# Performance work log

Measured on AMD Instinct MI355X. Metric: run time of the kernel, lower is better.

The kernel has to match this reference:

```python
import jax, jax.numpy as jnp
import numpy as np

B, L, D = 2, 2048, 2048
H, KV = 32, 8
HD = D // H          # 64
REP = H // KV        # 4


def setup_inputs() -> dict:
    key = jax.random.key(0)
    ks = jax.random.split(key, 6)
    x = jax.random.normal(ks[0], (B, L, D), dtype=jnp.float32)
    # weights stored [in, out] (transpose of torch Linear weight), scaled for stability
    wq = jax.random.normal(ks[1], (D, H * HD), dtype=jnp.float32) * 0.02
    wk = jax.random.normal(ks[2], (D, KV * HD), dtype=jnp.float32) * 0.02
    wv = jax.random.normal(ks[3], (D, KV * HD), dtype=jnp.float32) * 0.02
    wo = jax.random.normal(ks[4], (H * HD, D), dtype=jnp.float32) * 0.02
    # RoPE frequencies: freqs_cis = exp(i * pos * theta), theta_j = 10000^{-2j/HD}
    inv_freq = 1.0 / (10000.0 ** (jnp.arange(0, HD, 2, dtype=jnp.float32) / HD))  # [HD/2]
    angles = jnp.arange(L, dtype=jnp.float32)[:, None] * inv_freq[None, :]        # [L, HD/2]
    freqs_cos = jnp.cos(angles)
    freqs_sin = jnp.sin(angles)
    # additive causal mask [L, L] (prefill from start_pos=0)
    mask = jnp.where(jnp.tril(jnp.ones((L, L), dtype=bool)), 0.0, -jnp.inf).astype(jnp.float32)
    return {"x": x, "start_pos": 0, "freqs_cos": freqs_cos, "freqs_sin": freqs_sin,
            "mask": mask, "wq": wq, "wk": wk, "wv": wv, "wo": wo}


def _apply_rope(t, cos, sin):
    # t: [B, L, h, HD]; cos/sin: [L, HD/2] -> broadcast [1, L, 1, HD/2]
    tp = t.reshape(*t.shape[:-1], HD // 2, 2)
    a, b = tp[..., 0], tp[..., 1]
    c = cos[None, :, None, :]
    s = sin[None, :, None, :]
    ra = a * c - b * s
    rb = a * s + b * c
    return jnp.stack([ra, rb], axis=-1).reshape(t.shape)


def reference(x, start_pos, freqs_cos, freqs_sin, mask, wq, wk, wv, wo):
    xq = jnp.einsum('bld,de->ble', x, wq).reshape(B, L, H, HD)
    xk = jnp.einsum('bld,de->ble', x, wk).reshape(B, L, KV, HD)
    xv = jnp.einsum('bld,de->ble', x, wv).reshape(B, L, KV, HD)
    xq = _apply_rope(xq, freqs_cos, freqs_sin)
    xk = _apply_rope(xk, freqs_cos, freqs_sin)
    # (cache write of xk/xv is a dead side effect in the torch module; omitted)
    # GQA: query head (g*REP + r) attends to kv head g  == repeat_interleave semantics
    q = xq.transpose(0, 2, 1, 3).reshape(B, KV, REP, L, HD)  # [B,KV,REP,L,HD]
    k = xk.transpose(0, 2, 1, 3)                              # [B,KV,L,HD]
    v = xv.transpose(0, 2, 1, 3)
    scale = 1.0 / jnp.sqrt(jnp.float32(HD))
    scores = jnp.einsum('bgrld,bgmd->bgrlm', q, k) * scale + mask  # [B,KV,REP,L,L]
    attn = jax.nn.softmax(scores, axis=-1)
    out = jnp.einsum('bgrlm,bgmd->bgrld', attn, v)            # [B,KV,REP,L,HD]
    out = out.reshape(B, H, L, HD).transpose(0, 2, 1, 3).reshape(B, L, H * HD)
    return jnp.einsum('ble,ed->bld', out, wo)
```

## Files before the change

kernel.cpp:

```cpp
#include <hip/hip_runtime.h>
#include <hip/hip_bf16.h>
#include <math.h>

typedef __bf16 bf16_t;
typedef __bf16 bf16x8 __attribute__((ext_vector_type(8)));
typedef __bf16 bf16x4 __attribute__((ext_vector_type(4)));
typedef __bf16 bf16x2 __attribute__((ext_vector_type(2)));
typedef float  f32x4  __attribute__((ext_vector_type(4)));
typedef int    i32x4  __attribute__((ext_vector_type(4)));

#define B_  2
#define L_  2048
#define D_  2048
#define H_  32
#define KV_ 8
#define HD_ 64

static __device__ __forceinline__ void gload_lds16(const bf16_t* g, void* l)
{
    __builtin_amdgcn_global_load_lds(
        (const __attribute__((address_space(1))) void*)g,
        (__attribute__((address_space(3))) void*)l, 16, 0, 0);
}

static __device__ __forceinline__ int packbf(float a, float b)
{
    bf16x2 t; t[0] = (bf16_t)a; t[1] = (bf16_t)b;
    return __builtin_bit_cast(int, t);
}

static __device__ __forceinline__ void pl32(int& a, int& b)
{
    asm("v_permlane32_swap_b32 %0, %1" : "+v"(a), "+v"(b));
}
static __device__ __forceinline__ void pl16(int& a, int& b)
{
    asm("v_permlane16_swap_b32 %0, %1" : "+v"(a), "+v"(b));
}

#define WAITV4() asm volatile("s_waitcnt vmcnt(4)" ::: "memory")
#define WAITV2() asm volatile("s_waitcnt vmcnt(2)" ::: "memory")
#define WAITV0() asm volatile("s_waitcnt vmcnt(0)" ::: "memory")
#define WAITL0() asm volatile("s_waitcnt lgkmcnt(0)" ::: "memory")

__global__ void cast_f32_bf16(const float4* __restrict__ in,
                              bf16x4* __restrict__ out, int n4)
{
    const int i = blockIdx.x * 256 + threadIdx.x;
    if (i >= n4) return;
    const float4 v = in[i];
    bf16x4 o;
    o[0] = (bf16_t)v.x; o[1] = (bf16_t)v.y; o[2] = (bf16_t)v.z; o[3] = (bf16_t)v.w;
    out[i] = o;
}

template <typename InT>
__global__ void transpose_cast(const InT* __restrict__ in, bf16_t* __restrict__ out,
                               int R, int C)
{
    __shared__ bf16_t tile[32][33];
    const int bx = blockIdx.x * 32, by = blockIdx.y * 32;
    in  += (size_t)blockIdx.z * R * C;
    out += (size_t)blockIdx.z * R * C;
    const int tx = threadIdx.x, ty = threadIdx.y;
#pragma unroll
    for (int i = ty; i < 32; i += 8)
        tile[i][tx] = (bf16_t)(float)in[(size_t)(by + i) * C + bx + tx];
    __syncthreads();
#pragma unroll
    for (int i = ty; i < 32; i += 8)
        out[(size_t)(bx + i) * R + by + tx] = tile[tx][i];
}

#define FRAG(base, row, kk) \
    (*(const bf16x8*)((base) + (size_t)(row) * 128 + ((((kk) * 4 + quad) ^ sw8) << 4)))

#define STG_A(kt, h, buf) do {                                                        \
    gload_lds16(Ag + (size_t)((h) * 128)      * 2048 + (size_t)(kt) * 64,             \
                sdst + (buf) * 32768 + (h) * 16384);                                  \
    gload_lds16(Ag + (size_t)((h) * 128 + 64) * 2048 + (size_t)(kt) * 64,             \
                sdst + (buf) * 32768 + (h) * 16384 + 8192);                           \
} while (0)

#define STG_B(kt, h, buf) do {                                                        \
    gload_lds16(Bg + (size_t)((h) * 128)      * 2048 + (size_t)(kt) * 64,             \
                sdst + 65536 + (buf) * 32768 + (h) * 16384);                          \
    gload_lds16(Bg + (size_t)((h) * 128 + 64) * 2048 + (size_t)(kt) * 64,             \
                sdst + 65536 + (buf) * 32768 + (h) * 16384 + 8192);                   \
} while (0)

#define PHASE_SET(AB, BB, STG1, STG2, STG3, STG4, VM4)                                \
  {                                        \
    _Pragma("unroll") for (int m = 0; m < 4; m++) {                                   \
        Afr[m][0] = FRAG(AB, arow + m * 16, 0);                                       \
        Afr[m][1] = FRAG(AB, arow + m * 16, 1); }                                     \
    _Pragma("unroll") for (int n = 0; n < 2; n++) {                                   \
        B01[n][0] = FRAG(BB, brow + n * 16, 0);                                       \
        B01[n][1] = FRAG(BB, brow + n * 16, 1); }                                     \
    STG1;                                                                             \
    asm volatile("s_waitcnt lgkmcnt(8)" ::: "memory");                                \
    __builtin_amdgcn_s_barrier();                                                     \
    WAITL0();                                                                         \
    __builtin_amdgcn_s_setprio(1);                                                    \
    _Pragma("unroll") for (int m = 0; m < 4; m++)                                     \
      _Pragma("unroll") for (int n = 0; n < 2; n++)                                   \
        _Pragma("unroll") for (int kk = 0; kk < 2; kk++)                              \
          acc[m][n] = __builtin_amdgcn_mfma_f32_16x16x32_bf16(                        \
              Afr[m][kk], B01[n][kk], acc[m][n], 0, 0, 0);                            \
    __builtin_amdgcn_s_setprio(0);                                                    \
    __builtin_amdgcn_s_barrier();                                                     \
  }                                                                                   \
  {                                                 \
    _Pragma("unroll") for (int n = 0; n < 2; n++) {                                   \
        B23[n][0] = FRAG(BB, brow + (n + 2) * 16, 0);                                 \
        B23[n][1] = FRAG(BB, brow + (n + 2) * 16, 1); }                               \
    STG2;                                                                             \
    __builtin_amdgcn_s_barrier();                                                     \
    WAITL0();                                                                         \
    __builtin_amdgcn_s_setprio(1);                                                    \
    _Pragma("unroll") for (int m = 0; m < 4; m++)                                     \
      _Pragma("unroll") for (int n = 0; n < 2; n++)                                   \
        _Pragma("unroll") for (int kk = 0; kk < 2; kk++)                              \
          acc[m][n + 2] = __builtin_amdgcn_mfma_f32_16x16x32_bf16(                    \
              Afr[m][kk], B23[n][kk], acc[m][n + 2], 0, 0, 0);                        \
    __builtin_amdgcn_s_setprio(0);                                                    \
    __builtin_amdgcn_s_barrier();                                                     \
  }                                                                                   \
  {                                                 \
    _Pragma("unroll") for (int m = 0; m < 4; m++) {                                   \
        Afr[m][0] = FRAG(AB, arow + (m + 4) * 16, 0);                                 \
        Afr[m][1] = FRAG(AB, arow + (m + 4) * 16, 1); }                               \
    STG3;                                                                             \
    __builtin_amdgcn_s_barrier();                                                     \
    WAITL0();                                                                         \
    __builtin_amdgcn_s_setprio(1);                                                    \
    _Pragma("unroll") for (int m = 0; m < 4; m++)                                     \
      _Pragma("unroll") for (int n = 0; n < 2; n++)                                   \
        _Pragma("unroll") for (int kk = 0; kk < 2; kk++)                              \
          acc[m + 4][n + 2] = __builtin_amdgcn_mfma_f32_16x16x32_bf16(                \
              Afr[m][kk], B23[n][kk], acc[m + 4][n + 2], 0, 0, 0);                    \
    __builtin_amdgcn_s_setprio(0);                                                    \
    __builtin_amdgcn_s_barrier();                                                     \
  }                                                                                   \
  {                                        \
    STG4;                                                                             \
    VM4;                                                                              \
    __builtin_amdgcn_s_barrier();                                                     \
    __builtin_amdgcn_s_setprio(1);                                                    \
    _Pragma("unroll") for (int m = 0; m < 4; m++)                                     \
      _Pragma("unroll") for (int n = 0; n < 2; n++)                                   \
        _Pragma("unroll") for (int kk = 0; kk < 2; kk++)                              \
          acc[m + 4][n] = __builtin_amdgcn_mfma_f32_16x16x32_bf16(                    \
              Afr[m][kk], B01[n][kk], acc[m + 4][n], 0, 0, 0);                        \
    __builtin_amdgcn_s_setprio(0);                                                    \
    __builtin_amdgcn_s_barrier();                                                     \
  }

__global__ __launch_bounds__(512, 2) void gemm_qkv(
    const bf16_t* __restrict__ A,
    const bf16_t* __restrict__ BT,
    bf16_t* __restrict__ Qb, bf16_t* __restrict__ Kb, bf16_t* __restrict__ Vb)
{
    extern __shared__ __attribute__((aligned(16))) char DLDS[];
    constexpr int NITER = 2048 / 64 / 2;

    const int tid  = threadIdx.x;
    const int wave = tid >> 6;
    const int lane = tid & 63;
    const int quad = lane >> 4;
    const int l16  = lane & 15;
    const int wr   = wave >> 2;
    const int wc   = wave & 3;
    const int m0   = blockIdx.y * 256;
    const int n0   = blockIdx.x * 256;

    const int srow  = tid >> 3;
    const int swcol = ((tid & 7) ^ (srow & 7)) * 8;
    const bf16_t* Ag = A  + (size_t)(m0 + srow) * 2048 + swcol;
    const bf16_t* Bg = BT + (size_t)(n0 + srow) * 2048 + swcol;
    char* sdst = DLDS + tid * 16;

    const char* AB0 = DLDS;
    const char* AB1 = DLDS + 32768;
    const char* BB0 = DLDS + 65536;
    const char* BB1 = DLDS + 98304;
    const int sw8  = l16 & 7;
    const int arow = wr * 128 + l16;
    const int brow = wc * 64 + l16;

    f32x4 acc[8][4];
    const f32x4 zf = {0.f, 0.f, 0.f, 0.f};
#pragma unroll
    for (int i = 0; i < 8; i++)
#pragma unroll
        for (int j = 0; j < 4; j++) acc[i][j] = zf;

    bf16x8 Afr[4][2], B01[2][2], B23[2][2];

    STG_B(0, 0, 0); STG_B(0, 1, 0); STG_A(0, 0, 0); STG_A(0, 1, 0);
    STG_B(1, 0, 1); STG_B(1, 1, 1);
    WAITV4();
    __builtin_amdgcn_s_barrier();

    for (int i = 0; i < NITER; ++i) {
        const int t1 = 2 * i + 1;
        const int t2 = 2 * i + 2;
        const int t3 = 2 * i + 3;
        const bool more = (i + 1 < NITER);

        PHASE_SET(AB0, BB0,
                  STG_A(t1, 0, 1),
                  STG_A(t1, 1, 1),
                  if (more) STG_B(t2, 0, 0),
                  if (more) STG_B(t2, 1, 0),
                  if (more) { WAITV4(); } else { WAITV0(); })
        PHASE_SET(AB1, BB1,
                  if (more) STG_A(t2, 0, 0),
                  if (more) STG_A(t2, 1, 0),
                  if (more) STG_B(t3, 0, 1),
                  if (more) STG_B(t3, 1, 1),
                  WAITV4())
    }

    bf16_t* Cb; int ldc, coff; float cs = 1.f;
    if (n0 < 2048)      { Cb = Qb; ldc = 2048; coff = 0; }
    else if (n0 < 2560) { Cb = Kb; ldc = 512;  coff = 2048;
                          cs = 0.18033688011112042f; }
    else                { Cb = Vb; ldc = 512;  coff = 2560; }

#pragma unroll
    for (int mt = 0; mt < 8; mt++)
#pragma unroll
        for (int nt = 0; nt < 4; nt++)
#pragma unroll
            for (int r = 0; r < 4; r++) {
                const int row = m0 + wr * 128 + mt * 16 + quad * 4 + r;
                const int col = n0 + wc * 64 + nt * 16 + l16 - coff;
                Cb[(size_t)row * ldc + col] = (bf16_t)(acc[mt][nt][r] * cs);
            }
}

#undef FRAG
#undef STG_A
#undef STG_B
#undef PHASE_SET

#define OFRAG(base, row, kk) \
    (*(const bf16x8*)((base) + (size_t)(row) * 128 + ((((kk) * 4 + quad) ^ sw8) << 4)))

#define OSTG_A(kt, h, buf) do {                                                       \
    gload_lds16(Ag + (size_t)((h) * 128)      * 2048 + (size_t)(kt) * 64,             \
                adst + (buf) * 32768 + (h) * 16384);                                  \
    gload_lds16(Ag + (size_t)((h) * 128 + 64) * 2048 + (size_t)(kt) * 64,             \
                adst + (buf) * 32768 + (h) * 16384 + 8192);                           \
} while (0)

#define OSTG_B(kt, buf) do {                                                          \
    gload_lds16(Bg + (size_t)(kt) * 64,                       bdst + (buf) * 16384);  \
    gload_lds16(Bg + (size_t)64 * 2048 + (size_t)(kt) * 64,   bdst + (buf) * 16384 + 8192); \
} while (0)

#define OTILE(AB, BB, SA, SB, VMW)                                                    \
  {                                             \
    _Pragma("unroll") for (int m = 0; m < 4; m++) {                                   \
        Afr[m][0] = OFRAG(AB, arow + m * 16, 0);                                      \
        Afr[m][1] = OFRAG(AB, arow + m * 16, 1); }                                    \
    _Pragma("unroll") for (int n = 0; n < 2; n++) {                                   \
        Bfr[n][0] = OFRAG(BB, brow + n * 16, 0);                                      \
        Bfr[n][1] = OFRAG(BB, brow + n * 16, 1); }                                    \
    SA;                                                                               \
    asm volatile("s_waitcnt lgkmcnt(8)" ::: "memory");                                \
    __builtin_amdgcn_s_barrier();                                                     \
    WAITL0();                                                                         \
    __builtin_amdgcn_s_setprio(1);                                                    \
    _Pragma("unroll") for (int m = 0; m < 4; m++)                                     \
      _Pragma("unroll") for (int n = 0; n < 2; n++)                                   \
        _Pragma("unroll") for (int kk = 0; kk < 2; kk++)                              \
          acc[m][n] = __builtin_amdgcn_mfma_f32_16x16x32_bf16(                        \
              Afr[m][kk], Bfr[n][kk], acc[m][n], 0, 0, 0);                            \
    __builtin_amdgcn_s_setprio(0);                                                    \
    __builtin_amdgcn_s_barrier();                                                     \
  }                                                                                   \
  {                                \
    _Pragma("unroll") for (int m = 0; m < 4; m++) {                                   \
        Afr[m][0] = OFRAG(AB, arow + (m + 4) * 16, 0);                                \
        Afr[m][1] = OFRAG(AB, arow + (m + 4) * 16, 1); }                              \
    SB;                                                                               \
    VMW;                                                                              \
    __builtin_amdgcn_s_barrier();                                                     \
    WAITL0();                                                                         \
    __builtin_amdgcn_s_setprio(1);                                                    \
    _Pragma("unroll") for (int m = 0; m < 4; m++)                                     \
      _Pragma("unroll") for (int n = 0; n < 2; n++)                                   \
        _Pragma("unroll") for (int kk = 0; kk < 2; kk++)                              \
          acc[m + 4][n] = __builtin_amdgcn_mfma_f32_16x16x32_bf16(                    \
              Afr[m][kk], Bfr[n][kk], acc[m + 4][n], 0, 0, 0);                        \
    __builtin_amdgcn_s_setprio(0);                                                    \
    __builtin_amdgcn_s_barrier();                                                     \
  }

__global__ __launch_bounds__(512, 2) void gemm_out(
    const bf16_t* __restrict__ A,
    const bf16_t* __restrict__ BT,
    float* __restrict__ C)
{
    extern __shared__ __attribute__((aligned(16))) char DLDS[];
    constexpr int NITER = 2048 / 64 / 2;

    const int tid  = threadIdx.x;
    const int wave = tid >> 6;
    const int lane = tid & 63;
    const int quad = lane >> 4;
    const int l16  = lane & 15;
    const int wr   = wave >> 2;
    const int wc   = wave & 3;

    const int id   = blockIdx.x;
    const int w    = id >> 3;
    const int m0   = ((id & 7) * 2 + (w & 1)) * 256;
    const int n0   = (w >> 1) * 128;

    const int srow  = tid >> 3;
    const int swcol = ((tid & 7) ^ (srow & 7)) * 8;
    const bf16_t* Ag = A  + (size_t)(m0 + srow) * 2048 + swcol;
    const bf16_t* Bg = BT + (size_t)(n0 + srow) * 2048 + swcol;
    char* adst = DLDS + tid * 16;
    char* bdst = DLDS + 65536 + tid * 16;

    const char* AB0 = DLDS;
    const char* AB1 = DLDS + 32768;
    const char* BB0 = DLDS + 65536;
    const char* BB1 = DLDS + 81920;
    const int sw8  = l16 & 7;
    const int arow = wr * 128 + l16;
    const int brow = wc * 32 + l16;

    f32x4 acc[8][2];
    const f32x4 zf = {0.f, 0.f, 0.f, 0.f};
#pragma unroll
    for (int i = 0; i < 8; i++)
#pragma unroll
        for (int j = 0; j < 2; j++) acc[i][j] = zf;

    bf16x8 Afr[4][2], Bfr[2][2];

    OSTG_B(0, 0); OSTG_A(0, 0, 0); OSTG_A(0, 1, 0); OSTG_B(1, 1);
    WAITV2();
    __builtin_amdgcn_s_barrier();

    for (int i = 0; i < NITER; ++i) {
        const int v  = 2 * i + 1;
        const int t2 = 2 * i + 2;
        const int t3 = 2 * i + 3;
        const bool more = (i + 1 < NITER);

        OTILE(AB0, BB0,
              { OSTG_A(v, 0, 1); OSTG_A(v, 1, 1); },
              { if (more) OSTG_B(t2, 0); },
              if (more) { WAITV2(); } else { WAITV0(); })
        OTILE(AB1, BB1,
              { if (more) { OSTG_A(t2, 0, 0); OSTG_A(t2, 1, 0); } },
              { if (more) OSTG_B(t3, 1); },
              if (more) { WAITV2(); } else { WAITV0(); })
    }

#pragma unroll
    for (int mt = 0; mt < 8; mt++)
#pragma unroll
        for (int nt = 0; nt < 2; nt++)
#pragma unroll
            for (int r = 0; r < 4; r++) {
                const int row = m0 + wr * 128 + mt * 16 + quad * 4 + r;
                const int col = n0 + wc * 32 + nt * 16 + l16;
                C[(size_t)row * 2048 + col] = acc[mt][nt][r];
            }
}

#undef OFRAG
#undef OSTG_A
#undef OSTG_B
#undef OTILE

__global__ void rope_k(bf16_t* __restrict__ T, const float* __restrict__ fc,
                       const float* __restrict__ fs, int nheads, int total8)
{
    const int idx = blockIdx.x * 256 + threadIdx.x;
    if (idx >= total8) return;
    const int g  = idx & 7;
    const int t  = idx >> 3;
    const int h  = t % nheads;
    const int bl = t / nheads;
    const int l  = bl & (L_ - 1);
    const float4 c4 = *(const float4*)(fc + l * 32 + g * 4);
    const float4 s4 = *(const float4*)(fs + l * 32 + g * 4);
    const size_t off = ((size_t)bl * nheads + h) * 64 + g * 8;
    const bf16x8 v = *(const bf16x8*)(T + off);
    const float cc[4] = {c4.x, c4.y, c4.z, c4.w};
    const float ss[4] = {s4.x, s4.y, s4.z, s4.w};
    bf16x8 o;
#pragma unroll
    for (int p = 0; p < 4; p++) {
        const float a  = (float)v[2 * p];
        const float b2 = (float)v[2 * p + 1];
        o[2 * p]     = (bf16_t)(a * cc[p] - b2 * ss[p]);
        o[2 * p + 1] = (bf16_t)(a * ss[p] + b2 * cc[p]);
    }
    *(bf16x8*)(T + off) = o;
}

__global__ __launch_bounds__(256, 2) void attn_k(
    const bf16_t* __restrict__ Q,
    const bf16_t* __restrict__ Kc,
    const bf16_t* __restrict__ VT,
    bf16_t* __restrict__ Ob)
{
    __shared__ __attribute__((aligned(16))) char LDS[32768];
    float* OL = (float*)LDS;
    float* LR = (float*)(LDS + 17408);

    const int tid  = threadIdx.x;
    const int wave = tid >> 6;
    const int lane = tid & 63;
    const int quad = lane >> 4;
    const int l16  = lane & 15;

    const int id   = blockIdx.y * 16 + blockIdx.x;
    const int c    = (id >> 3) & 15;
    const int bh   = (id & 7) * 8 + (id >> 7);
    const int bb   = bh >> 5;
    const int h    = bh & 31;
    const int kvh  = h >> 2;
    const size_t bbL = (size_t)bb * L_;

    const int schunk = ((lane & 3) ^ ((lane >> 3) & 3)) * 8;
    const int sw16   = ((l16 >> 1) & 3) * 16;

    const bf16_t* Kg = Kc + bbL * (KV_ * HD_) + kvh * HD_;
    const bf16_t* Vg = VT + (size_t)(bb * KV_ + kvh) * HD_ * L_;
    const bf16_t* KgL = Kg + (size_t)(wave * 32 + (lane >> 2)) * (KV_ * HD_) + schunk;
    const bf16_t* VgL = Vg + (size_t)(lane >> 2) * L_ + wave * 32 + schunk;
    char* kdst0 = (char*)LDS + wave * 2048 + (lane << 4);
    char* vdst0 = (char*)LDS + 16384 + wave * 4096 + (lane << 4);

    const f32x4 zf = {0.f, 0.f, 0.f, 0.f};

    for (int half = 0; half < 2; ++half) {
        const int j     = half ? c : 31 - c;
        const int qbase = j * 64;
        const int nkt   = (j + 2) >> 1;

        bf16x8 qf[4][2];
#pragma unroll
        for (int qt = 0; qt < 4; qt++) {
            const bf16_t* qrow = Q + ((bbL + qbase + qt * 16 + l16) * H_ + h) * HD_;
            qf[qt][0] = *(const bf16x8*)(qrow + quad * 8);
            qf[qt][1] = *(const bf16x8*)(qrow + 32 + quad * 8);
        }

        f32x4 acc[4][4];
#pragma unroll
        for (int mt = 0; mt < 4; mt++)
#pragma unroll
            for (int qt = 0; qt < 4; qt++) acc[mt][qt] = zf;
        float lacc[4] = {0.f, 0.f, 0.f, 0.f};

#pragma unroll
        for (int cc = 0; cc < 2; cc++)
#pragma unroll
            for (int sub = 0; sub < 2; sub++)
                gload_lds16(KgL + (size_t)(sub * 16) * (KV_ * HD_) + cc * 32,
                            kdst0 + cc * 8192 + sub * 1024);
#pragma unroll
        for (int sub = 0; sub < 4; sub++)
            gload_lds16(VgL + (size_t)(sub * 16) * L_, vdst0 + sub * 1024);

        for (int kt = 0; kt < nkt; kt++) {
            WAITV0();

            const char* Kld = LDS;
            const char* Vld = LDS + 16384;

            bf16x8 kf[2][2];
#pragma unroll
            for (int t = 0; t < 2; t++)
#pragma unroll
                for (int cc = 0; cc < 2; cc++)
                    kf[t][cc] = *(const bf16x8*)(Kld + cc * 8192 +
                        (wave * 32 + t * 16 + l16) * 64 + ((quad * 16) ^ sw16));

            bf16x8 vf[4];
#pragma unroll
            for (int mt = 0; mt < 4; mt++)
                vf[mt] = *(const bf16x8*)(Vld + wave * 4096 +
                    (mt * 16 + l16) * 64 + ((quad * 16) ^ sw16));

            WAITL0();

            if (kt + 1 < nkt) {
                const int ktb = (kt + 1) * 128;
#pragma unroll
                for (int cc = 0; cc < 2; cc++)
#pragma unroll
                    for (int sub = 0; sub < 2; sub++)
                        gload_lds16(KgL + (size_t)(ktb + sub * 16) * (KV_ * HD_) + cc * 32,
                                    kdst0 + cc * 8192 + sub * 1024);
#pragma unroll
                for (int sub = 0; sub < 4; sub++)
                    gload_lds16(VgL + (size_t)(sub * 16) * L_ + ktb,
                                vdst0 + sub * 1024);
            }

            f32x4 st[2][4];
            __builtin_amdgcn_s_setprio(1);
#pragma unroll
            for (int t = 0; t < 2; t++)
#pragma unroll
                for (int qt = 0; qt < 4; qt++) {
                    f32x4 s = __builtin_amdgcn_mfma_f32_16x16x32_bf16(
                        kf[t][0], qf[qt][0], zf, 0, 0, 0);
                    st[t][qt] = __builtin_amdgcn_mfma_f32_16x16x32_bf16(
                        kf[t][1], qf[qt][1], s, 0, 0, 0);
                }
            __builtin_amdgcn_s_setprio(0);

            if (kt == nkt - 1) {
                const int kq = kt * 128 + wave * 32 + quad * 4 - qbase - l16;
#pragma unroll
                for (int t = 0; t < 2; t++)
#pragma unroll
                    for (int qt = 0; qt < 4; qt++)
#pragma unroll
                        for (int r = 0; r < 4; r++)
                            st[t][qt][r] = (kq + t * 16 - qt * 16 + r <= 0)
                                         ? st[t][qt][r] : -__builtin_inff();
            }

            int pk[2][4][2];
#pragma unroll
            for (int t = 0; t < 2; t++)
#pragma unroll
                for (int qt = 0; qt < 4; qt++) {
                    const float e0 = __builtin_amdgcn_exp2f(st[t][qt][0]);
                    const float e1 = __builtin_amdgcn_exp2f(st[t][qt][1]);
                    const float e2 = __builtin_amdgcn_exp2f(st[t][qt][2]);
                    const float e3 = __builtin_amdgcn_exp2f(st[t][qt][3]);
                    lacc[qt] += (e0 + e1) + (e2 + e3);
                    pk[t][qt][0] = packbf(e0, e1);
                    pk[t][qt][1] = packbf(e2, e3);
                }

#pragma unroll
            for (int qt = 0; qt < 4; qt++) {
                int a0 = pk[0][qt][0], b0 = pk[1][qt][0];
                pl32(a0, b0); pl16(a0, b0);
                int a1 = pk[0][qt][1], b1 = pk[1][qt][1];
                pl32(a1, b1); pl16(a1, b1);
                i32x4 bi;
                bi[0] = a0; bi[1] = a1; bi[2] = b0; bi[3] = b1;
                const bf16x8 pb = __builtin_bit_cast(bf16x8, bi);
                __builtin_amdgcn_s_setprio(1);
#pragma unroll
                for (int mt = 0; mt < 4; mt++)
                    acc[mt][qt] = __builtin_amdgcn_mfma_f32_16x16x32_bf16(
                        vf[mt], pb, acc[mt][qt], 0, 0, 0);
                __builtin_amdgcn_s_setprio(0);
            }
        }

        float lw[4];
#pragma unroll
        for (int qt = 0; qt < 4; qt++) {
            float v = lacc[qt];
            v += __shfl_xor(v, 16);
            v += __shfl_xor(v, 32);
            lw[qt] = v;
        }

        __syncthreads();

        if (quad == 0)
#pragma unroll
            for (int qt = 0; qt < 4; qt++)
                LR[(wave * 4 + qt) * 16 + l16] = lw[qt];

#pragma unroll
        for (int p = 0; p < 4; p++) {
#pragma unroll
            for (int qt = 0; qt < 4; qt++) {
                if (((qt - wave) & 3) == p) {
#pragma unroll
                    for (int mt = 0; mt < 4; mt++) {
                        float* a = OL + (qt * 16 + l16) * 68 + mt * 16 + quad * 4;
                        if (p == 0) *(f32x4*)a = acc[mt][qt];
                        else        *(f32x4*)a = *(f32x4*)a + acc[mt][qt];
                    }
                }
            }
            __syncthreads();
        }

        const float ls = LR[(0 * 4 + wave) * 16 + l16] + LR[(1 * 4 + wave) * 16 + l16]
                       + LR[(2 * 4 + wave) * 16 + l16] + LR[(3 * 4 + wave) * 16 + l16];
        const float inv = 1.f / ls;
        bf16_t* orow = Ob + ((bbL + qbase + wave * 16 + l16) * H_ + h) * HD_;
#pragma unroll
        for (int j2 = 0; j2 < 4; j2++) {
            const f32x4 v = *(const f32x4*)(OL + (wave * 16 + l16) * 68 + quad * 16 + j2 * 4);
            bf16x4 o;
#pragma unroll
            for (int i = 0; i < 4; i++) o[i] = (bf16_t)(v[i] * inv);
            *(bf16x4*)(orow + quad * 16 + j2 * 4) = o;
        }
        __syncthreads();
    }
}

extern "C" void kernel_launch(void* const* d_in, const int* in_sizes, int n_in,
                              void* d_out, int out_size, void* d_ws, size_t ws_size,
                              hipStream_t stream)
{
    (void)in_sizes; (void)n_in; (void)out_size; (void)ws_size;
    const float* xf = (const float*)d_in[0];
    const float* fc = (const float*)d_in[2];
    const float* fs = (const float*)d_in[3];
    const float* wq = (const float*)d_in[5];
    const float* wk = (const float*)d_in[6];
    const float* wv = (const float*)d_in[7];
    const float* wo = (const float*)d_in[8];
    float* out = (float*)d_out;

    char* ws = (char*)d_ws;
    bf16_t* xb   = (bf16_t*)(ws);
    bf16_t* Qb   = (bf16_t*)(ws + (16ull << 20));
    bf16_t* Kb   = (bf16_t*)(ws + (32ull << 20));
    bf16_t* Vb   = (bf16_t*)(ws + (36ull << 20));
    bf16_t* VTb  = (bf16_t*)(ws + (40ull << 20));
    bf16_t* Oa   = (bf16_t*)(ws + (44ull << 20));
    bf16_t* Wqkv = (bf16_t*)(ws + (60ull << 20));
    bf16_t* WoT  = (bf16_t*)(ws + (72ull << 20));

    cast_f32_bf16<<<8192, 256, 0, stream>>>((const float4*)xf, (bf16x4*)xb,
                                            B_ * L_ * D_ / 4);

    const dim3 tb(32, 8);
    transpose_cast<float><<<dim3(64, 64, 1), tb, 0, stream>>>(wq, Wqkv, 2048, 2048);
    transpose_cast<float><<<dim3(16, 64, 1), tb, 0, stream>>>(wk, Wqkv + 2048ull * 2048, 2048, 512);
    transpose_cast<float><<<dim3(16, 64, 1), tb, 0, stream>>>(wv, Wqkv + 2560ull * 2048, 2048, 512);
    transpose_cast<float><<<dim3(64, 64, 1), tb, 0, stream>>>(wo, WoT, 2048, 2048);

    gemm_qkv<<<dim3(12, 16), 512, 131072, stream>>>(xb, Wqkv, Qb, Kb, Vb);

    rope_k<<<4096, 256, 0, stream>>>(Qb, fc, fs, 32, B_ * L_ * 32 * 8);
    rope_k<<<1024, 256, 0, stream>>>(Kb, fc, fs, 8, B_ * L_ * 8 * 8);

    transpose_cast<bf16_t><<<dim3(16, 64, 2), tb, 0, stream>>>(Vb, VTb, 2048, 512);

    attn_k<<<dim3(16, 64), 256, 0, stream>>>(Qb, Kb, VTb, Oa);

    gemm_out<<<dim3(256), 512, 98304, stream>>>(Oa, WoT, out);
}
```

Before: 305.0 us.

## Retile QKV GEMM to 256x192 tiles, fuse prep and RoPE launches

The QKV projection GEMM moves from 256x256 tiles on a 12x16 grid (192 blocks) to 256x192 tiles on 256 blocks. The intent is to fill all compute units of the MI355X and cut wave-quantization idle time; the B-operand staging and the LDS size shrink to match. The weight transpose-casts and the x cast are merged into one prep launch, and the Q and K RoPE launches are merged into one, to reduce launch overhead. In exchange, the epilogue now routes each output element to Q, K or V with per-element branching, and the K-scale is applied by column.

```diff
diff --git a/kernel.cpp b/kernel.cpp
--- a/kernel.cpp
+++ b/kernel.cpp
@@ -38,20 +38,49 @@
     asm("v_permlane16_swap_b32 %0, %1" : "+v"(a), "+v"(b));
 }
 
-#define WAITV4() asm volatile("s_waitcnt vmcnt(4)" ::: "memory")
+#define WAITV3() asm volatile("s_waitcnt vmcnt(3)" ::: "memory")
 #define WAITV2() asm volatile("s_waitcnt vmcnt(2)" ::: "memory")
 #define WAITV0() asm volatile("s_waitcnt vmcnt(0)" ::: "memory")
 #define WAITL0() asm volatile("s_waitcnt lgkmcnt(0)" ::: "memory")
 
-__global__ void cast_f32_bf16(const float4* __restrict__ in,
-                              bf16x4* __restrict__ out, int n4)
-{
-    const int i = blockIdx.x * 256 + threadIdx.x;
-    if (i >= n4) return;
-    const float4 v = in[i];
-    bf16x4 o;
-    o[0] = (bf16_t)v.x; o[1] = (bf16_t)v.y; o[2] = (bf16_t)v.z; o[3] = (bf16_t)v.w;
-    out[i] = o;
+__global__ void prep_k(const float* __restrict__ wq, const float* __restrict__ wk,
+                       const float* __restrict__ wv, const float* __restrict__ wo,
+                       const float* __restrict__ xf,
+                       bf16_t* __restrict__ Wqkv, bf16_t* __restrict__ WoT,
+                       bf16_t* __restrict__ xb)
+{
+    __shared__ bf16_t tile[32][33];
+    const int z  = blockIdx.z;
+    const int tx = threadIdx.x, ty = threadIdx.y;
+
+    if (z == 4) {
+        const size_t base = ((size_t)(blockIdx.y * 64 + blockIdx.x) * 256
+                             + ty * 32 + tx) * 8;
+        const float4 v0 = *(const float4*)(xf + base);
+        const float4 v1 = *(const float4*)(xf + base + 4);
+        bf16x8 o;
+        o[0] = (bf16_t)v0.x; o[1] = (bf16_t)v0.y; o[2] = (bf16_t)v0.z; o[3] = (bf16_t)v0.w;
+        o[4] = (bf16_t)v1.x; o[5] = (bf16_t)v1.y; o[6] = (bf16_t)v1.z; o[7] = (bf16_t)v1.w;
+        *(bf16x8*)(xb + base) = o;
+        return;
+    }
+
+    const float* in; bf16_t* out; int C;
+    if (z == 0)      { in = wq; out = Wqkv;                  C = 2048; }
+    else if (z == 1) { in = wk; out = Wqkv + 2048ull * 2048; C = 512;  }
+    else if (z == 2) { in = wv; out = Wqkv + 2560ull * 2048; C = 512;  }
+    else             { in = wo; out = WoT;                   C = 2048; }
+
+    const int bx = blockIdx.x * 32, by = blockIdx.y * 32;
+    if (bx >= C) return;
+    const int R = 2048;
+#pragma unroll
+    for (int i = ty; i < 32; i += 8)
+        tile[i][tx] = (bf16_t)in[(size_t)(by + i) * C + bx + tx];
+    __syncthreads();
+#pragma unroll
+    for (int i = ty; i < 32; i += 8)
+        out[(size_t)(bx + i) * R + by + tx] = tile[tx][i];
 }
 
 template <typename InT>
@@ -82,22 +111,19 @@
                 sdst + (buf) * 32768 + (h) * 16384 + 8192);                           \
 } while (0)
 
-#define STG_B(kt, h, buf) do {                                                        \
-    gload_lds16(Bg + (size_t)((h) * 128)      * 2048 + (size_t)(kt) * 64,             \
-                sdst + 65536 + (buf) * 32768 + (h) * 16384);                          \
-    gload_lds16(Bg + (size_t)((h) * 128 + 64) * 2048 + (size_t)(kt) * 64,             \
-                sdst + 65536 + (buf) * 32768 + (h) * 16384 + 8192);                   \
-} while (0)
-
-#define PHASE_SET(AB, BB, STG1, STG2, STG3, STG4, VM4)                                \
-  {                                        \
+#define STG_BU(kt, u, buf)                                                            \
+    gload_lds16(Bg + (size_t)((u) * 64) * 2048 + (size_t)(kt) * 64,                   \
+                sdst + 65536 + (buf) * 24576 + (u) * 8192)
+
+#define QTILE(AB, BB, S1, S2, S3, S4, VMW)                                            \
+  {                                  \
     _Pragma("unroll") for (int m = 0; m < 4; m++) {                                   \
         Afr[m][0] = FRAG(AB, arow + m * 16, 0);                                       \
         Afr[m][1] = FRAG(AB, arow + m * 16, 1); }                                     \
     _Pragma("unroll") for (int n = 0; n < 2; n++) {                                   \
         B01[n][0] = FRAG(BB, brow + n * 16, 0);                                       \
         B01[n][1] = FRAG(BB, brow + n * 16, 1); }                                     \
-    STG1;                                                                             \
+    S1;                                                                               \
     asm volatile("s_waitcnt lgkmcnt(8)" ::: "memory");                                \
     __builtin_amdgcn_s_barrier();                                                     \
     WAITL0();                                                                         \
@@ -110,41 +136,38 @@
     __builtin_amdgcn_s_setprio(0);                                                    \
     __builtin_amdgcn_s_barrier();                                                     \
   }                                                                                   \
-  {                                                 \
-    _Pragma("unroll") for (int n = 0; n < 2; n++) {                                   \
-        B23[n][0] = FRAG(BB, brow + (n + 2) * 16, 0);                                 \
-        B23[n][1] = FRAG(BB, brow + (n + 2) * 16, 1); }                               \
-    STG2;                                                                             \
+  {                                              \
+    B2f[0] = FRAG(BB, brow + 32, 0);                                                  \
+    B2f[1] = FRAG(BB, brow + 32, 1);                                                  \
+    S2;                                                                               \
     __builtin_amdgcn_s_barrier();                                                     \
     WAITL0();                                                                         \
     __builtin_amdgcn_s_setprio(1);                                                    \
     _Pragma("unroll") for (int m = 0; m < 4; m++)                                     \
-      _Pragma("unroll") for (int n = 0; n < 2; n++)                                   \
-        _Pragma("unroll") for (int kk = 0; kk < 2; kk++)                              \
-          acc[m][n + 2] = __builtin_amdgcn_mfma_f32_16x16x32_bf16(                    \
-              Afr[m][kk], B23[n][kk], acc[m][n + 2], 0, 0, 0);                        \
+      _Pragma("unroll") for (int kk = 0; kk < 2; kk++)                                \
+          acc[m][2] = __builtin_amdgcn_mfma_f32_16x16x32_bf16(                        \
+              Afr[m][kk], B2f[kk], acc[m][2], 0, 0, 0);                               \
     __builtin_amdgcn_s_setprio(0);                                                    \
     __builtin_amdgcn_s_barrier();                                                     \
   }                                                                                   \
-  {                                                 \
+  {                                            \
     _Pragma("unroll") for (int m = 0; m < 4; m++) {                                   \
         Afr[m][0] = FRAG(AB, arow + (m + 4) * 16, 0);                                 \
         Afr[m][1] = FRAG(AB, arow + (m + 4) * 16, 1); }                               \
-    STG3;                                                                             \
+    S3;                                                                               \
     __builtin_amdgcn_s_barrier();                                                     \
     WAITL0();                                                                         \
     __builtin_amdgcn_s_setprio(1);                                                    \
     _Pragma("unroll") for (int m = 0; m < 4; m++)                                     \
-      _Pragma("unroll") for (int n = 0; n < 2; n++)                                   \
-        _Pragma("unroll") for (int kk = 0; kk < 2; kk++)                              \
-          acc[m + 4][n + 2] = __builtin_amdgcn_mfma_f32_16x16x32_bf16(                \
-              Afr[m][kk], B23[n][kk], acc[m + 4][n + 2], 0, 0, 0);                    \
+      _Pragma("unroll") for (int kk = 0; kk < 2; kk++)                                \
+          acc[m + 4][2] = __builtin_amdgcn_mfma_f32_16x16x32_bf16(                    \
+              Afr[m][kk], B2f[kk], acc[m + 4][2], 0, 0, 0);                           \
     __builtin_amdgcn_s_setprio(0);                                                    \
     __builtin_amdgcn_s_barrier();                                                     \
   }                                                                                   \
-  {                                        \
-    STG4;                                                                             \
-    VM4;                                                                              \
+  {                                \
+    S4;                                                                               \
+    VMW;                                                                              \
     __builtin_amdgcn_s_barrier();                                                     \
     __builtin_amdgcn_s_setprio(1);                                                    \
     _Pragma("unroll") for (int m = 0; m < 4; m++)                                     \
@@ -171,8 +194,11 @@
     const int l16  = lane & 15;
     const int wr   = wave >> 2;
     const int wc   = wave & 3;
-    const int m0   = blockIdx.y * 256;
-    const int n0   = blockIdx.x * 256;
+
+    const int id   = blockIdx.x;
+    const int w    = id >> 3;
+    const int m0   = ((id & 7) * 2 + (w & 1)) * 256;
+    const int n0   = (w >> 1) * 192;
 
     const int srow  = tid >> 3;
     const int swcol = ((tid & 7) ^ (srow & 7)) * 8;
@@ -183,23 +209,24 @@
     const char* AB0 = DLDS;
     const char* AB1 = DLDS + 32768;
     const char* BB0 = DLDS + 65536;
-    const char* BB1 = DLDS + 98304;
+    const char* BB1 = DLDS + 90112;
     const int sw8  = l16 & 7;
     const int arow = wr * 128 + l16;
-    const int brow = wc * 64 + l16;
-
-    f32x4 acc[8][4];
+    const int brow = wc * 48 + l16;
+
+    f32x4 acc[8][3];
     const f32x4 zf = {0.f, 0.f, 0.f, 0.f};
 #pragma unroll
     for (int i = 0; i < 8; i++)
 #pragma unroll
-        for (int j = 0; j < 4; j++) acc[i][j] = zf;
-
-    bf16x8 Afr[4][2], B01[2][2], B23[2][2];
-
-    STG_B(0, 0, 0); STG_B(0, 1, 0); STG_A(0, 0, 0); STG_A(0, 1, 0);
-    STG_B(1, 0, 1); STG_B(1, 1, 1);
-    WAITV4();
+        for (int j = 0; j < 3; j++) acc[i][j] = zf;
+
+    bf16x8 Afr[4][2], B01[2][2], B2f[2];
+
+    STG_BU(0, 0, 0); STG_BU(0, 1, 0); STG_BU(0, 2, 0);
+    STG_A(0, 0, 0);  STG_A(0, 1, 0);
+    STG_BU(1, 0, 1); STG_BU(1, 1, 1); STG_BU(1, 2, 1);
+    WAITV3();
     __builtin_amdgcn_s_barrier();
 
     for (int i = 0; i < NITER; ++i) {
@@ -208,42 +235,43 @@
         const int t3 = 2 * i + 3;
         const bool more = (i + 1 < NITER);
 
-        PHASE_SET(AB0, BB0,
-                  STG_A(t1, 0, 1),
-                  STG_A(t1, 1, 1),
-                  if (more) STG_B(t2, 0, 0),
-                  if (more) STG_B(t2, 1, 0),
-                  if (more) { WAITV4(); } else { WAITV0(); })
-        PHASE_SET(AB1, BB1,
-                  if (more) STG_A(t2, 0, 0),
-                  if (more) STG_A(t2, 1, 0),
-                  if (more) STG_B(t3, 0, 1),
-                  if (more) STG_B(t3, 1, 1),
-                  WAITV4())
+        QTILE(AB0, BB0,
+              STG_A(t1, 0, 1),
+              STG_A(t1, 1, 1),
+              if (more) { STG_BU(t2, 0, 0); STG_BU(t2, 1, 0); },
+              if (more) { STG_BU(t2, 2, 0); },
+              if (more) { WAITV3(); } else { WAITV0(); })
+        QTILE(AB1, BB1,
+              if (more) STG_A(t2, 0, 0),
+              if (more) STG_A(t2, 1, 0),
+              if (more) { STG_BU(t3, 0, 1); STG_BU(t3, 1, 1); },
+              if (more) { STG_BU(t3, 2, 1); },
+              if (more) { WAITV3(); } else { WAITV0(); })
     }
 
-    bf16_t* Cb; int ldc, coff; float cs = 1.f;
-    if (n0 < 2048)      { Cb = Qb; ldc = 2048; coff = 0; }
-    else if (n0 < 2560) { Cb = Kb; ldc = 512;  coff = 2048;
-                          cs = 0.18033688011112042f; }
-    else                { Cb = Vb; ldc = 512;  coff = 2560; }
-
+    const float cs = 0.18033688011112042f;
 #pragma unroll
     for (int mt = 0; mt < 8; mt++)
 #pragma unroll
-        for (int nt = 0; nt < 4; nt++)
+        for (int nt = 0; nt < 3; nt++)
 #pragma unroll
             for (int r = 0; r < 4; r++) {
-                const int row = m0 + wr * 128 + mt * 16 + quad * 4 + r;
-                const int col = n0 + wc * 64 + nt * 16 + l16 - coff;
-                Cb[(size_t)row * ldc + col] = (bf16_t)(acc[mt][nt][r] * cs);
+                const int row  = m0 + wr * 128 + mt * 16 + quad * 4 + r;
+                const int gcol = n0 + wc * 48 + nt * 16 + l16;
+                const float v  = acc[mt][nt][r];
+                if (gcol < 2048)
+                    Qb[(size_t)row * 2048 + gcol] = (bf16_t)v;
+                else if (gcol < 2560)
+                    Kb[(size_t)row * 512 + (gcol - 2048)] = (bf16_t)(v * cs);
+                else
+                    Vb[(size_t)row * 512 + (gcol - 2560)] = (bf16_t)v;
             }
 }
 
 #undef FRAG
 #undef STG_A
-#undef STG_B
-#undef PHASE_SET
+#undef STG_BU
+#undef QTILE
 
 #define OFRAG(base, row, kk) \
     (*(const bf16x8*)((base) + (size_t)(row) * 128 + ((((kk) * 4 + quad) ^ sw8) << 4)))
@@ -381,11 +409,14 @@
 #undef OSTG_B
 #undef OTILE
 
-__global__ void rope_k(bf16_t* __restrict__ T, const float* __restrict__ fc,
-                       const float* __restrict__ fs, int nheads, int total8)
-{
-    const int idx = blockIdx.x * 256 + threadIdx.x;
-    if (idx >= total8) return;
+__global__ void rope2_k(bf16_t* __restrict__ Qb, bf16_t* __restrict__ Kb,
+                        const float* __restrict__ fc, const float* __restrict__ fs)
+{
+    int idx = blockIdx.x * 256 + threadIdx.x;
+    bf16_t* T; int nheads;
+    if (idx < B_ * L_ * 32 * 8) { T = Qb; nheads = 32; }
+    else { T = Kb; nheads = 8; idx -= B_ * L_ * 32 * 8; }
+
     const int g  = idx & 7;
     const int t  = idx >> 3;
     const int h  = t % nheads;
@@ -639,19 +670,12 @@
     bf16_t* Wqkv = (bf16_t*)(ws + (60ull << 20));
     bf16_t* WoT  = (bf16_t*)(ws + (72ull << 20));
 
-    cast_f32_bf16<<<8192, 256, 0, stream>>>((const float4*)xf, (bf16x4*)xb,
-                                            B_ * L_ * D_ / 4);
-
     const dim3 tb(32, 8);
-    transpose_cast<float><<<dim3(64, 64, 1), tb, 0, stream>>>(wq, Wqkv, 2048, 2048);
-    transpose_cast<float><<<dim3(16, 64, 1), tb, 0, stream>>>(wk, Wqkv + 2048ull * 2048, 2048, 512);
-    transpose_cast<float><<<dim3(16, 64, 1), tb, 0, stream>>>(wv, Wqkv + 2560ull * 2048, 2048, 512);
-    transpose_cast<float><<<dim3(64, 64, 1), tb, 0, stream>>>(wo, WoT, 2048, 2048);
-
-    gemm_qkv<<<dim3(12, 16), 512, 131072, stream>>>(xb, Wqkv, Qb, Kb, Vb);
-
-    rope_k<<<4096, 256, 0, stream>>>(Qb, fc, fs, 32, B_ * L_ * 32 * 8);
-    rope_k<<<1024, 256, 0, stream>>>(Kb, fc, fs, 8, B_ * L_ * 8 * 8);
+    prep_k<<<dim3(64, 64, 5), tb, 0, stream>>>(wq, wk, wv, wo, xf, Wqkv, WoT, xb);
+
+    gemm_qkv<<<dim3(256), 512, 114688, stream>>>(xb, Wqkv, Qb, Kb, Vb);
+
+    rope2_k<<<5120, 256, 0, stream>>>(Qb, Kb, fc, fs);
 
     transpose_cast<bf16_t><<<dim3(16, 64, 2), tb, 0, stream>>>(Vb, VTb, 2048, 512);
 
```

Result: faster. 296.6 us (-2.8%).
